# Kernel optimization log

Hardware: AMD Instinct MI355X
Metric: run time of the kernel (lower is better)

Reference implementation:

```python
import jax, jax.numpy as jnp
import numpy as np

N_A, N_B = 50000, 20000   # authors, teams
E0, E1, E2 = 600000, 300000, 300000  # coauthor(A->A), writes(A->B), influences(B->A)
D = 128                   # in_feats = out_feats


def setup_inputs() -> dict:
    key = jax.random.key(0)
    ks = jax.random.split(key, 12)
    h_A = jax.random.normal(ks[0], (N_A, D), jnp.float32)
    h_B = jax.random.normal(ks[1], (N_B, D), jnp.float32)
    W0 = jax.random.normal(ks[2], (D, D), jnp.float32) * 0.05
    W1 = jax.random.normal(ks[3], (D, D), jnp.float32) * 0.05
    W2 = jax.random.normal(ks[4], (D, D), jnp.float32) * 0.05
    b0 = jnp.zeros((D,), jnp.float32)
    b1 = jnp.zeros((D,), jnp.float32)
    b2 = jnp.zeros((D,), jnp.float32)
    src0 = jax.random.randint(ks[5], (E0,), 0, N_A)
    dst0 = jax.random.randint(ks[6], (E0,), 0, N_A)
    src1 = jax.random.randint(ks[7], (E1,), 0, N_A)
    dst1 = jax.random.randint(ks[8], (E1,), 0, N_B)
    src2 = jax.random.randint(ks[9], (E2,), 0, N_B)
    dst2 = jax.random.randint(ks[10], (E2,), 0, N_A)
    return dict(h_A=h_A, h_B=h_B, W0=W0, b0=b0, W1=W1, b1=b1, W2=W2, b2=b2,
                src0=src0, dst0=dst0, src1=src1, dst1=dst1, src2=src2, dst2=dst2)


def _graph_conv(x_src, W, b, src, dst, n_dst):
    """DGL GraphConv, norm='both': out = D_dst^{-1/2} A D_src^{-1/2} (X W) + b."""
    n_src = x_src.shape[0]
    ones = jnp.ones(src.shape[0], x_src.dtype)
    deg_out = jnp.clip(jax.ops.segment_sum(ones, src, num_segments=n_src), 1.0)
    deg_in = jnp.clip(jax.ops.segment_sum(ones, dst, num_segments=n_dst), 1.0)
    m = (x_src @ W) * (deg_out ** -0.5)[:, None]          # [n_src, D]
    agg = jax.ops.segment_sum(m[src], dst, num_segments=n_dst)  # [n_dst, D]
    return agg * (deg_in ** -0.5)[:, None] + b


def reference(h_A, h_B, W0, b0, W1, b1, W2, b2, src0, dst0, src1, dst1, src2, dst2):
    # HeteroGraphConv(aggregate='sum'): sum per-relation GraphConv outputs per dst ntype.
    out_A = (_graph_conv(h_A, W0, b0, src0, dst0, N_A)
             + _graph_conv(h_B, W2, b2, src2, dst2, N_A))
    out_B = _graph_conv(h_A, W1, b1, src1, dst1, N_B)
    # every ntype present in h receives an output, so no passthrough branch fires
    return out_A, out_B
```

## Files before the change

kernel.cpp:

```cpp
#include <hip/hip_runtime.h>

#define NA 50000
#define NB 20000
#define NE0 600000
#define NE1 300000
#define NE2 300000
#define DD 128
#define DEG_TOT (4 * NA + 2 * NB)
#define SUB 32768
#define PER 18750


typedef short bf16x8 __attribute__((ext_vector_type(8)));
typedef float f32x4 __attribute__((ext_vector_type(4)));

__device__ __forceinline__ unsigned short f2bf(float f) {
    union { float f; unsigned int u; } v; v.f = f;
    unsigned int r = v.u + 0x7fffu + ((v.u >> 16) & 1u);
    return (unsigned short)(r >> 16);
}
__device__ __forceinline__ float bf2f(unsigned int u16) {
    union { float f; unsigned int u; } v; v.u = u16 << 16;
    return v.f;
}
__device__ __forceinline__ float lo2f(unsigned int u) {
    union { float f; unsigned int u; } v; v.u = u << 16;
    return v.f;
}
__device__ __forceinline__ float hi2f(unsigned int u) {
    union { float f; unsigned int u; } v; v.u = u & 0xffff0000u;
    return v.f;
}

__global__ __launch_bounds__(1024) void hist_kernel(
    const int* __restrict__ s0, const int* __restrict__ d0,
    const int* __restrict__ s1, const int* __restrict__ d1,
    const int* __restrict__ s2, const int* __restrict__ d2,
    unsigned int* __restrict__ Pd,
    int* __restrict__ rank0, int* __restrict__ rank1, int* __restrict__ rank2)
{
    __shared__ unsigned int h32[SUB / 2];
    const int cfg = blockIdx.z;
    const int En[6] = {NE0, NE0, NE1, NE1, NE2, NE2};
    const int Kn[6] = {NA, NA, NA, NB, NB, NA};
    const int Gn[6] = {32, 32, 16, 16, 16, 16};
    const int Po[6] = {0, 1600000, 3200000, 4000000, 4320000, 4640000};
    int E = En[cfg], K = Kn[cfg], G = Gn[cfg];
    int sub = blockIdx.x, g = blockIdx.y;
    int nsub = (K + SUB - 1) / SUB;
    if (sub >= nsub || g >= G) return;
    const int* keys = cfg == 0 ? s0 : cfg == 1 ? d0 : cfg == 2 ? s1
                    : cfg == 3 ? d1 : cfg == 4 ? s2 : d2;
    int* rk = cfg == 1 ? rank0 : cfg == 3 ? rank1 : cfg == 5 ? rank2 : (int*)0;
    int lo = sub * SUB;
    int hi = min(K, lo + SUB);
    int cnt = hi - lo;
    for (int i = threadIdx.x; i < SUB / 2; i += 1024) h32[i] = 0;
    __syncthreads();
    int e1 = min(E, g * PER + PER);
    for (int e = g * PER + threadIdx.x; e < e1; e += 1024) {
        int k = keys[e];
        if (k >= lo && k < hi) {
            int kk = k - lo;
            unsigned sh = (kk & 1) << 4;
            unsigned old = atomicAdd(&h32[kk >> 1], 1u << sh);
            if (rk) rk[e] = (int)((old >> sh) & 0xffffu);
        }
    }
    __syncthreads();
    unsigned int* outp = Pd + ((Po[cfg] + g * K + lo) >> 1);
    for (int i = threadIdx.x; i < cnt / 2; i += 1024) outp[i] = h32[i];
}

__global__ __launch_bounds__(256) void reduce_kernel(
    const unsigned short* __restrict__ P16, int* __restrict__ ideg,
    float* __restrict__ rdeg)
{
    int i = blockIdx.x * 256 + threadIdx.x;
    if (i >= DEG_TOT) return;
    int h, k;
    if      (i < NA)            { h = 0; k = i; }
    else if (i < 2 * NA)        { h = 1; k = i - NA; }
    else if (i < 3 * NA)        { h = 2; k = i - 2 * NA; }
    else if (i < 3 * NA + NB)   { h = 3; k = i - 3 * NA; }
    else if (i < 3 * NA + 2*NB) { h = 4; k = i - 3 * NA - NB; }
    else                        { h = 5; k = i - 3 * NA - 2 * NB; }
    const int Po[6] = {0, 1600000, 3200000, 4000000, 4320000, 4640000};
    const int Gn[6] = {32, 32, 16, 16, 16, 16};
    const int Kn[6] = {NA, NA, NA, NB, NB, NA};
    const unsigned short* p = P16 + Po[h] + k;
    int K = Kn[h], G = Gn[h], s = 0;
    for (int g = 0; g < G; ++g) s += p[g * K];
    ideg[i] = s;
    rdeg[i] = rsqrtf(fmaxf((float)s, 1.f));
}

__global__ __launch_bounds__(256) void scan_reduce(
    const int* __restrict__ ideg, int* __restrict__ spart)
{
    __shared__ int lds[256];
    int y = blockIdx.y;
    const int off[3] = {NA, 3 * NA, 3 * NA + 2 * NB};
    const int nn[3]  = {NA, NB, NA};
    int n = nn[y];
    int b = blockIdx.x, t = threadIdx.x;
    if (b * 1024 >= n) return;
    const int* deg = ideg + off[y];
    int base = b * 1024 + t * 4;
    int s = 0;
    #pragma unroll
    for (int k = 0; k < 4; ++k) { int i = base + k; if (i < n) s += deg[i]; }
    lds[t] = s; __syncthreads();
    for (int o = 128; o > 0; o >>= 1) {
        if (t < o) lds[t] += lds[t + o];
        __syncthreads();
    }
    if (t == 0) spart[y * 64 + b] = lds[0];
}

__global__ void spine_kernel(int* __restrict__ spart) {
    int w = threadIdx.x >> 6, lane = threadIdx.x & 63;
    const int nblk[3] = {49, 20, 49};
    int n = nblk[w];
    int* p = spart + w * 64;
    int orig = (lane < n) ? p[lane] : 0;
    int v = orig;
    #pragma unroll
    for (int o = 1; o < 64; o <<= 1) {
        int u = __shfl_up(v, o);
        if (lane >= o) v += u;
    }
    if (lane < n) p[lane] = v - orig;
}

__global__ __launch_bounds__(256) void scan_final(
    const int* __restrict__ ideg, const int* __restrict__ spart,
    int* __restrict__ rp)
{
    __shared__ int lds[256];
    int y = blockIdx.y;
    const int off[3] = {NA, 3 * NA, 3 * NA + 2 * NB};
    const int nn[3]  = {NA, NB, NA};
    const int ro[3]  = {0, NA, NA + NB};
    int n = nn[y];
    int b = blockIdx.x, t = threadIdx.x;
    if (b * 1024 >= n) return;
    const int* deg = ideg + off[y];
    int* rowptr = rp + ro[y];
    int base = b * 1024 + t * 4;
    int v[4]; int tsum = 0;
    #pragma unroll
    for (int k = 0; k < 4; ++k) {
        v[k] = (base + k < n) ? deg[base + k] : 0;
        tsum += v[k];
    }
    lds[t] = tsum; __syncthreads();
    for (int o = 1; o < 256; o <<= 1) {
        int x = (t >= o) ? lds[t - o] : 0;
        __syncthreads();
        lds[t] += x;
        __syncthreads();
    }
    int run = lds[t] - tsum + spart[y * 64 + b];
    #pragma unroll
    for (int k = 0; k < 4; ++k) {
        if (base + k < n) rowptr[base + k] = run;
        run += v[k];
    }
}

__global__ __launch_bounds__(256) void offsets_kernel(
    const unsigned short* __restrict__ P16, const int* __restrict__ rp,
    int* __restrict__ O)
{
    int i = blockIdx.x * 256 + threadIdx.x;
    if (i >= 2 * NA + NB) return;
    int pbase, obase, G, K, d, run;
    if (i < NA)           { pbase = 1600000; obase = 0;       G = 32; K = NA; d = i;           run = rp[d]; }
    else if (i < NA + NB) { pbase = 4000000; obase = 1600000; G = 16; K = NB; d = i - NA;      run = rp[NA + d]; }
    else                  { pbase = 4640000; obase = 1920000; G = 16; K = NA; d = i - NA - NB; run = rp[NA + NB + d]; }
    const unsigned short* p = P16 + pbase + d;
    int* o = O + obase + d;
    for (int g = 0; g < G; ++g) {
        int t = p[g * K];
        o[g * K] = run;
        run += t;
    }
}

__global__ __launch_bounds__(512) void place_parallel(
    const int* __restrict__ s0, const int* __restrict__ d0,
    const int* __restrict__ s1, const int* __restrict__ d1,
    const int* __restrict__ s2, const int* __restrict__ d2,
    const int* __restrict__ O,
    const int* __restrict__ rank0, const int* __restrict__ rank1,
    const int* __restrict__ rank2,
    int* __restrict__ csr0, int* __restrict__ csr1, int* __restrict__ csr2)
{
    int z = blockIdx.z;
    const int En[3] = {NE0, NE1, NE2};
    const int Kn[3] = {NA, NB, NA};
    const int Oo[3] = {0, 1600000, 1920000};
    int E = En[z], K = Kn[z];
    const int* src = z == 0 ? s0 : z == 1 ? s1 : s2;
    const int* dst = z == 0 ? d0 : z == 1 ? d1 : d2;
    const int* rk  = z == 0 ? rank0 : z == 1 ? rank1 : rank2;
    int* csr = z == 0 ? csr0 : z == 1 ? csr1 : csr2;
    const int* off = O + Oo[z];
    int e = blockIdx.x * 512 + threadIdx.x;
    if (e >= E) return;
    int d = dst[e];
    int g = e / PER;
    int pos = off[g * K + d] + rk[e];
    csr[pos] = src[e];
}

__global__ __launch_bounds__(256) void wt_kernel(
    const float* __restrict__ W0, const float* __restrict__ W1,
    const float* __restrict__ W2, unsigned short* __restrict__ Wt)
{
    int i = blockIdx.x * 256 + threadIdx.x;
    if (i >= 3 * DD * DD) return;
    int w = i >> 14, r = i & (DD * DD - 1);
    int c = r >> 7, k = r & (DD - 1);
    const float* W = (w == 0) ? W0 : ((w == 1) ? W1 : W2);
    Wt[i] = f2bf(W[k * DD + c]);
}

__global__ __launch_bounds__(256) void gemm_all(
    const float* __restrict__ hA, const float* __restrict__ hB,
    const unsigned short* __restrict__ Wt, const float* __restrict__ rdeg,
    unsigned short* __restrict__ mA0, unsigned short* __restrict__ mA1,
    unsigned short* __restrict__ mB2)
{
    int wid  = threadIdx.x >> 6;
    int lane = threadIdx.x & 63;
    int quad = lane >> 4;
    int l16  = lane & 15;

    if (blockIdx.x < 782) {
        int base = blockIdx.x * 64 + wid * 16;
        if (base >= NA) return;
        int arow = base + l16;
        if (arow >= NA) arow = NA - 1;
        bf16x8 a[4];
        #pragma unroll
        for (int kk = 0; kk < 4; ++kk) {
            const float4* p = (const float4*)(hA + (size_t)arow * DD + kk * 32 + quad * 8);
            float4 u = p[0], w = p[1];
            bf16x8 t;
            t[0] = (short)f2bf(u.x); t[1] = (short)f2bf(u.y);
            t[2] = (short)f2bf(u.z); t[3] = (short)f2bf(u.w);
            t[4] = (short)f2bf(w.x); t[5] = (short)f2bf(w.y);
            t[6] = (short)f2bf(w.z); t[7] = (short)f2bf(w.w);
            a[kk] = t;
        }
        float rs0[4], rs1[4]; int orow0 = base + quad * 4;
        #pragma unroll
        for (int r = 0; r < 4; ++r) {
            int orow = orow0 + r; int c = orow < NA ? orow : 0;
            rs0[r] = rdeg[c]; rs1[r] = rdeg[2 * NA + c];
        }
        #pragma unroll
        for (int ct = 0; ct < 8; ++ct) {
            f32x4 acc0 = {0.f, 0.f, 0.f, 0.f};
            f32x4 acc1 = {0.f, 0.f, 0.f, 0.f};
            const unsigned short* wp = Wt + (size_t)(ct * 16 + l16) * DD + quad * 8;
            #pragma unroll
            for (int kk = 0; kk < 4; ++kk) {
                bf16x8 b0 = *(const bf16x8*)(wp + kk * 32);
                bf16x8 b1 = *(const bf16x8*)(wp + 16384 + kk * 32);
                acc0 = __builtin_amdgcn_mfma_f32_16x16x32_bf16(a[kk], b0, acc0, 0, 0, 0);
                acc1 = __builtin_amdgcn_mfma_f32_16x16x32_bf16(a[kk], b1, acc1, 0, 0, 0);
            }
            #pragma unroll
            for (int r = 0; r < 4; ++r) {
                int orow = orow0 + r;
                if (orow < NA) {
                    mA0[(size_t)orow * DD + ct * 16 + l16] = f2bf(acc0[r] * rs0[r]);
                    mA1[(size_t)orow * DD + ct * 16 + l16] = f2bf(acc1[r] * rs1[r]);
                }
            }
        }
    } else {
        int base = (blockIdx.x - 782) * 64 + wid * 16;
        if (base >= NB) return;
        int arow = base + l16;
        if (arow >= NB) arow = NB - 1;
        bf16x8 a[4];
        #pragma unroll
        for (int kk = 0; kk < 4; ++kk) {
            const float4* p = (const float4*)(hB + (size_t)arow * DD + kk * 32 + quad * 8);
            float4 u = p[0], w = p[1];
            bf16x8 t;
            t[0] = (short)f2bf(u.x); t[1] = (short)f2bf(u.y);
            t[2] = (short)f2bf(u.z); t[3] = (short)f2bf(u.w);
            t[4] = (short)f2bf(w.x); t[5] = (short)f2bf(w.y);
            t[6] = (short)f2bf(w.z); t[7] = (short)f2bf(w.w);
            a[kk] = t;
        }
        float rs[4]; int orow0 = base + quad * 4;
        #pragma unroll
        for (int r = 0; r < 4; ++r) {
            int orow = orow0 + r;
            rs[r] = rdeg[3 * NA + NB + (orow < NB ? orow : 0)];
        }
        #pragma unroll
        for (int ct = 0; ct < 8; ++ct) {
            f32x4 acc = {0.f, 0.f, 0.f, 0.f};
            const unsigned short* wp = Wt + 32768 + (size_t)(ct * 16 + l16) * DD + quad * 8;
            #pragma unroll
            for (int kk = 0; kk < 4; ++kk) {
                bf16x8 b = *(const bf16x8*)(wp + kk * 32);
                acc = __builtin_amdgcn_mfma_f32_16x16x32_bf16(a[kk], b, acc, 0, 0, 0);
            }
            #pragma unroll
            for (int r = 0; r < 4; ++r) {
                int orow = orow0 + r;
                if (orow < NB)
                    mB2[(size_t)orow * DD + ct * 16 + l16] = f2bf(acc[r] * rs[r]);
            }
        }
    }
}

__device__ __forceinline__ void gather_rel(
    const char* __restrict__ Mb, const int* __restrict__ csr,
    int st, int n, int lane, unsigned laneoff, float& o0, float& o1)
{
    for (int ch = 0; ch < n; ch += 64) {
        int m = n - ch; if (m > 64) m = 64;
        int idx = csr[st + ch + (lane < m ? lane : m - 1)];
        int j = 0;
        for (; j + 4 <= m; j += 4) {
            int sA = __shfl(idx, j);
            int sB = __shfl(idx, j + 1);
            int sC = __shfl(idx, j + 2);
            int sD = __shfl(idx, j + 3);
            unsigned uA = *(const unsigned*)(Mb + (((unsigned)sA << 8) + laneoff));
            unsigned uB = *(const unsigned*)(Mb + (((unsigned)sB << 8) + laneoff));
            unsigned uC = *(const unsigned*)(Mb + (((unsigned)sC << 8) + laneoff));
            unsigned uD = *(const unsigned*)(Mb + (((unsigned)sD << 8) + laneoff));
            o0 += lo2f(uA); o1 += hi2f(uA);
            o0 += lo2f(uB); o1 += hi2f(uB);
            o0 += lo2f(uC); o1 += hi2f(uC);
            o0 += lo2f(uD); o1 += hi2f(uD);
        }
        for (; j < m; ++j) {
            int s = __shfl(idx, j);
            unsigned u = *(const unsigned*)(Mb + (((unsigned)s << 8) + laneoff));
            o0 += lo2f(u); o1 += hi2f(u);
        }
    }
}

__global__ __launch_bounds__(256) void gather_all(
    const unsigned short* __restrict__ mA0, const unsigned short* __restrict__ mA1,
    const unsigned short* __restrict__ mB2,
    const int* __restrict__ csr0, const int* __restrict__ csr1,
    const int* __restrict__ csr2,
    const int* __restrict__ rp, const int* __restrict__ ideg,
    const float* __restrict__ rdeg,
    const float* __restrict__ b0, const float* __restrict__ b1,
    const float* __restrict__ b2,
    float* __restrict__ out)
{
    int wid = threadIdx.x >> 6, lane = threadIdx.x & 63;
    unsigned laneoff = (unsigned)lane * 4u;
    int col = lane * 2;

    if (blockIdx.x < 12500) {
        int d = blockIdx.x * 4 + wid;
        float a0 = 0.f, a1 = 0.f, c0 = 0.f, c1 = 0.f;
        gather_rel((const char*)mA0, csr0, rp[d], ideg[NA + d], lane, laneoff, a0, a1);
        gather_rel((const char*)mB2, csr2, rp[NA + NB + d], ideg[3 * NA + 2 * NB + d],
                   lane, laneoff, c0, c1);
        float r0 = rdeg[NA + d], r2 = rdeg[3 * NA + 2 * NB + d];
        float2 o;
        o.x = a0 * r0 + c0 * r2 + b0[col]     + b2[col];
        o.y = a1 * r0 + c1 * r2 + b0[col + 1] + b2[col + 1];
        *(float2*)(out + (size_t)d * DD + col) = o;
    } else {
        int d = (blockIdx.x - 12500) * 4 + wid;
        float a0 = 0.f, a1 = 0.f;
        gather_rel((const char*)mA1, csr1, rp[NA + d], ideg[3 * NA + d],
                   lane, laneoff, a0, a1);
        float r1 = rdeg[3 * NA + d];
        float2 o;
        o.x = a0 * r1 + b1[col];
        o.y = a1 * r1 + b1[col + 1];
        *(float2*)(out + (size_t)(NA + d) * DD + col) = o;
    }
}

extern "C" void kernel_launch(void* const* d_in, const int* in_sizes, int n_in,
                              void* d_out, int out_size, void* d_ws, size_t ws_size,
                              hipStream_t stream) {
    const float* hA = (const float*)d_in[0];
    const float* hB = (const float*)d_in[1];
    const float* W0 = (const float*)d_in[2];
    const float* b0 = (const float*)d_in[3];
    const float* W1 = (const float*)d_in[4];
    const float* b1 = (const float*)d_in[5];
    const float* W2 = (const float*)d_in[6];
    const float* b2 = (const float*)d_in[7];
    const int* s0 = (const int*)d_in[8];
    const int* d0 = (const int*)d_in[9];
    const int* s1 = (const int*)d_in[10];
    const int* d1 = (const int*)d_in[11];
    const int* s2 = (const int*)d_in[12];
    const int* d2 = (const int*)d_in[13];
    float* out = (float*)d_out;
    char* ws = (char*)d_ws;

    unsigned short* mA0 = (unsigned short*)(ws + 0);
    unsigned short* mA1 = (unsigned short*)(ws + 12800000);
    unsigned short* mB2 = (unsigned short*)(ws + 25600000);
    unsigned short* P16 = (unsigned short*)(ws + 0);
    unsigned int*   Pd  = (unsigned int*)(ws + 0);
    int*   O            = (int*)  (ws + 10880000);
    unsigned short* Wt  = (unsigned short*)(ws + 30720000);
    float* rdeg         = (float*)(ws + 30818304);
    int*   ideg         = (int*)  (ws + 31778304);
    int*   rp           = (int*)  (ws + 32738304);
    int*   spart        = (int*)  (ws + 33218304);
    int*   rank0        = (int*)  (ws + 33219328);
    int*   rank1        = (int*)  (ws + 35619328);
    int*   rank2        = (int*)  (ws + 36819328);
    int*   csr0         = (int*)  (ws + 38019328);
    int*   csr1         = (int*)  (ws + 40419328);
    int*   csr2         = (int*)  (ws + 41619328);

    hist_kernel<<<dim3(2, 32, 6), 1024, 0, stream>>>(s0, d0, s1, d1, s2, d2,
                                                     Pd, rank0, rank1, rank2);
    reduce_kernel<<<(DEG_TOT + 255) / 256, 256, 0, stream>>>(P16, ideg, rdeg);

    scan_reduce<<<dim3(49, 3), 256, 0, stream>>>(ideg, spart);
    spine_kernel<<<1, 192, 0, stream>>>(spart);
    scan_final<<<dim3(49, 3), 256, 0, stream>>>(ideg, spart, rp);

    offsets_kernel<<<(2 * NA + NB + 255) / 256, 256, 0, stream>>>(P16, rp, O);
    place_parallel<<<dim3((NE0 + 511) / 512, 1, 3), 512, 0, stream>>>(
        s0, d0, s1, d1, s2, d2, O, rank0, rank1, rank2, csr0, csr1, csr2);

    wt_kernel<<<(3 * DD * DD + 255) / 256, 256, 0, stream>>>(W0, W1, W2, Wt);
    gemm_all<<<782 + 313, 256, 0, stream>>>(hA, hB, Wt, rdeg, mA0, mA1, mB2);

    gather_all<<<12500 + 5000, 256, 0, stream>>>(mA0, mA1, mB2,
        csr0, csr1, csr2, rp, ideg, rdeg, b0, b1, b2, out);
}
```

Measured before the change: 264.7 us.

## Fuse preprocessing kernels and widen gather loads to 16-byte rows per quarter-wave

Folds the weight transpose/convert into an extra z-slice of the histogram kernel. It merges degree reduction with the scan partial sums, and merges the scan spine and per-group offsets into the final scan, cutting the launch count from nine to five. The gather kernel now has each 16-lane quarter of a wave load a full 256-byte bf16 row with uint4 loads, processing four edges at once, then reduces the quarters with shuffles. This trades fewer launches and wider memory transactions for a redundant spine prefix in every block and the extra cross-lane reduction.

Result: slower. 276.9 us (+4.6%).

```diff
diff --git a/kernel.cpp b/kernel.cpp
--- a/kernel.cpp
+++ b/kernel.cpp
@@ -19,10 +19,6 @@
     unsigned int r = v.u + 0x7fffu + ((v.u >> 16) & 1u);
     return (unsigned short)(r >> 16);
 }
-__device__ __forceinline__ float bf2f(unsigned int u16) {
-    union { float f; unsigned int u; } v; v.u = u16 << 16;
-    return v.f;
-}
 __device__ __forceinline__ float lo2f(unsigned int u) {
     union { float f; unsigned int u; } v; v.u = u << 16;
     return v.f;
@@ -37,10 +33,22 @@
     const int* __restrict__ s1, const int* __restrict__ d1,
     const int* __restrict__ s2, const int* __restrict__ d2,
     unsigned int* __restrict__ Pd,
-    int* __restrict__ rank0, int* __restrict__ rank1, int* __restrict__ rank2)
+    int* __restrict__ rank0, int* __restrict__ rank1, int* __restrict__ rank2,
+    const float* __restrict__ W0, const float* __restrict__ W1,
+    const float* __restrict__ W2, unsigned short* __restrict__ Wt)
 {
     __shared__ unsigned int h32[SUB / 2];
     const int cfg = blockIdx.z;
+    if (cfg == 6) {
+        int flat = blockIdx.y * 2 + blockIdx.x;
+        if (flat >= 48) return;
+        int i = flat * 1024 + threadIdx.x;
+        int w = i >> 14, r = i & (DD * DD - 1);
+        int c = r >> 7, k = r & (DD - 1);
+        const float* W = (w == 0) ? W0 : ((w == 1) ? W1 : W2);
+        Wt[i] = f2bf(W[k * DD + c]);
+        return;
+    }
     const int En[6] = {NE0, NE0, NE1, NE1, NE2, NE2};
     const int Kn[6] = {NA, NA, NA, NB, NB, NA};
     const int Gn[6] = {32, 32, 16, 16, 16, 16};
@@ -72,81 +80,67 @@
     for (int i = threadIdx.x; i < cnt / 2; i += 1024) outp[i] = h32[i];
 }
 
-__global__ __launch_bounds__(256) void reduce_kernel(
+__global__ __launch_bounds__(256) void reduce2(
     const unsigned short* __restrict__ P16, int* __restrict__ ideg,
-    float* __restrict__ rdeg)
-{
-    int i = blockIdx.x * 256 + threadIdx.x;
-    if (i >= DEG_TOT) return;
-    int h, k;
-    if      (i < NA)            { h = 0; k = i; }
-    else if (i < 2 * NA)        { h = 1; k = i - NA; }
-    else if (i < 3 * NA)        { h = 2; k = i - 2 * NA; }
-    else if (i < 3 * NA + NB)   { h = 3; k = i - 3 * NA; }
-    else if (i < 3 * NA + 2*NB) { h = 4; k = i - 3 * NA - NB; }
-    else                        { h = 5; k = i - 3 * NA - 2 * NB; }
+    float* __restrict__ rdeg, int* __restrict__ spart)
+{
+    __shared__ int lds[256];
+    const int y = blockIdx.y;
+    const int Ro[6] = {0, NA, 2 * NA, 3 * NA, 3 * NA + NB, 3 * NA + 2 * NB};
+    const int Kr[6] = {NA, NA, NA, NB, NB, NA};
+    const int Gr[6] = {32, 32, 16, 16, 16, 16};
     const int Po[6] = {0, 1600000, 3200000, 4000000, 4320000, 4640000};
-    const int Gn[6] = {32, 32, 16, 16, 16, 16};
-    const int Kn[6] = {NA, NA, NA, NB, NB, NA};
-    const unsigned short* p = P16 + Po[h] + k;
-    int K = Kn[h], G = Gn[h], s = 0;
-    for (int g = 0; g < G; ++g) s += p[g * K];
-    ideg[i] = s;
-    rdeg[i] = rsqrtf(fmaxf((float)s, 1.f));
-}
-
-__global__ __launch_bounds__(256) void scan_reduce(
-    const int* __restrict__ ideg, int* __restrict__ spart)
+    int K = Kr[y], G = Gr[y];
+    int b = blockIdx.x, t = threadIdx.x;
+    if (b * 1024 >= K) return;
+    int base = b * 1024 + t * 4;
+    int tsum = 0;
+    #pragma unroll
+    for (int k = 0; k < 4; ++k) {
+        int key = base + k;
+        if (key < K) {
+            const unsigned short* p = P16 + Po[y] + key;
+            int s = 0;
+            for (int g = 0; g < G; ++g) s += p[g * K];
+            ideg[Ro[y] + key] = s;
+            rdeg[Ro[y] + key] = rsqrtf(fmaxf((float)s, 1.f));
+            tsum += s;
+        }
+    }
+    if (y == 1 || y == 3 || y == 5) {
+        int slot = (y - 1) >> 1;
+        lds[t] = tsum; __syncthreads();
+        for (int o = 128; o > 0; o >>= 1) {
+            if (t < o) lds[t] += lds[t + o];
+            __syncthreads();
+        }
+        if (t == 0) spart[slot * 64 + b] = lds[0];
+    }
+}
+
+__global__ __launch_bounds__(256) void scan_final2(
+    const int* __restrict__ ideg, const int* __restrict__ spart,
+    const unsigned short* __restrict__ P16,
+    int* __restrict__ rp, int* __restrict__ O)
 {
     __shared__ int lds[256];
-    int y = blockIdx.y;
-    const int off[3] = {NA, 3 * NA, 3 * NA + 2 * NB};
-    const int nn[3]  = {NA, NB, NA};
-    int n = nn[y];
+    const int y = blockIdx.y;
+    const int off[3]   = {NA, 3 * NA, 3 * NA + 2 * NB};
+    const int nn[3]    = {NA, NB, NA};
+    const int ro[3]    = {0, NA, NA + NB};
+    const int pbase[3] = {1600000, 4000000, 4640000};
+    const int obase[3] = {0, 1600000, 1920000};
+    const int Gd[3]    = {32, 16, 16};
+    int n = nn[y], K = n, G = Gd[y];
     int b = blockIdx.x, t = threadIdx.x;
     if (b * 1024 >= n) return;
+    int lane = t & 63;
+
+    int pv = (lane < b) ? spart[y * 64 + lane] : 0;
+    #pragma unroll
+    for (int o = 32; o > 0; o >>= 1) pv += __shfl_xor(pv, o);
+
     const int* deg = ideg + off[y];
-    int base = b * 1024 + t * 4;
-    int s = 0;
-    #pragma unroll
-    for (int k = 0; k < 4; ++k) { int i = base + k; if (i < n) s += deg[i]; }
-    lds[t] = s; __syncthreads();
-    for (int o = 128; o > 0; o >>= 1) {
-        if (t < o) lds[t] += lds[t + o];
-        __syncthreads();
-    }
-    if (t == 0) spart[y * 64 + b] = lds[0];
-}
-
-__global__ void spine_kernel(int* __restrict__ spart) {
-    int w = threadIdx.x >> 6, lane = threadIdx.x & 63;
-    const int nblk[3] = {49, 20, 49};
-    int n = nblk[w];
-    int* p = spart + w * 64;
-    int orig = (lane < n) ? p[lane] : 0;
-    int v = orig;
-    #pragma unroll
-    for (int o = 1; o < 64; o <<= 1) {
-        int u = __shfl_up(v, o);
-        if (lane >= o) v += u;
-    }
-    if (lane < n) p[lane] = v - orig;
-}
-
-__global__ __launch_bounds__(256) void scan_final(
-    const int* __restrict__ ideg, const int* __restrict__ spart,
-    int* __restrict__ rp)
-{
-    __shared__ int lds[256];
-    int y = blockIdx.y;
-    const int off[3] = {NA, 3 * NA, 3 * NA + 2 * NB};
-    const int nn[3]  = {NA, NB, NA};
-    const int ro[3]  = {0, NA, NA + NB};
-    int n = nn[y];
-    int b = blockIdx.x, t = threadIdx.x;
-    if (b * 1024 >= n) return;
-    const int* deg = ideg + off[y];
-    int* rowptr = rp + ro[y];
     int base = b * 1024 + t * 4;
     int v[4]; int tsum = 0;
     #pragma unroll
@@ -161,30 +155,22 @@
         lds[t] += x;
         __syncthreads();
     }
-    int run = lds[t] - tsum + spart[y * 64 + b];
+    int run = lds[t] - tsum + pv;
+    int* rowptr = rp + ro[y];
+    const unsigned short* pb = P16 + pbase[y];
+    int* ob = O + obase[y];
     #pragma unroll
     for (int k = 0; k < 4; ++k) {
-        if (base + k < n) rowptr[base + k] = run;
-        run += v[k];
-    }
-}
-
-__global__ __launch_bounds__(256) void offsets_kernel(
-    const unsigned short* __restrict__ P16, const int* __restrict__ rp,
-    int* __restrict__ O)
-{
-    int i = blockIdx.x * 256 + threadIdx.x;
-    if (i >= 2 * NA + NB) return;
-    int pbase, obase, G, K, d, run;
-    if (i < NA)           { pbase = 1600000; obase = 0;       G = 32; K = NA; d = i;           run = rp[d]; }
-    else if (i < NA + NB) { pbase = 4000000; obase = 1600000; G = 16; K = NB; d = i - NA;      run = rp[NA + d]; }
-    else                  { pbase = 4640000; obase = 1920000; G = 16; K = NA; d = i - NA - NB; run = rp[NA + NB + d]; }
-    const unsigned short* p = P16 + pbase + d;
-    int* o = O + obase + d;
-    for (int g = 0; g < G; ++g) {
-        int t = p[g * K];
-        o[g * K] = run;
-        run += t;
+        int key = base + k;
+        if (key < n) {
+            rowptr[key] = run;
+            int r2 = run;
+            for (int g = 0; g < G; ++g) {
+                ob[g * K + key] = r2;
+                r2 += pb[g * K + key];
+            }
+            run += v[k];
+        }
     }
 }
 
@@ -213,18 +199,6 @@
     int g = e / PER;
     int pos = off[g * K + d] + rk[e];
     csr[pos] = src[e];
-}
-
-__global__ __launch_bounds__(256) void wt_kernel(
-    const float* __restrict__ W0, const float* __restrict__ W1,
-    const float* __restrict__ W2, unsigned short* __restrict__ Wt)
-{
-    int i = blockIdx.x * 256 + threadIdx.x;
-    if (i >= 3 * DD * DD) return;
-    int w = i >> 14, r = i & (DD * DD - 1);
-    int c = r >> 7, k = r & (DD - 1);
-    const float* W = (w == 0) ? W0 : ((w == 1) ? W1 : W2);
-    Wt[i] = f2bf(W[k * DD + c]);
 }
 
 __global__ __launch_bounds__(256) void gemm_all(
@@ -324,32 +298,42 @@
     }
 }
 
-__device__ __forceinline__ void gather_rel(
+__device__ __forceinline__ void acc8(float* o, uint4 u) {
+    o[0] += lo2f(u.x); o[1] += hi2f(u.x);
+    o[2] += lo2f(u.y); o[3] += hi2f(u.y);
+    o[4] += lo2f(u.z); o[5] += hi2f(u.z);
+    o[6] += lo2f(u.w); o[7] += hi2f(u.w);
+}
+__device__ __forceinline__ void gather_rel4(
     const char* __restrict__ Mb, const int* __restrict__ csr,
-    int st, int n, int lane, unsigned laneoff, float& o0, float& o1)
+    int st, int n, int lane, int q, unsigned laneoff, float* o)
 {
     for (int ch = 0; ch < n; ch += 64) {
         int m = n - ch; if (m > 64) m = 64;
         int idx = csr[st + ch + (lane < m ? lane : m - 1)];
         int j = 0;
-        for (; j + 4 <= m; j += 4) {
-            int sA = __shfl(idx, j);
-            int sB = __shfl(idx, j + 1);
-            int sC = __shfl(idx, j + 2);
-            int sD = __shfl(idx, j + 3);
-            unsigned uA = *(const unsigned*)(Mb + (((unsigned)sA << 8) + laneoff));
-            unsigned uB = *(const unsigned*)(Mb + (((unsigned)sB << 8) + laneoff));
-            unsigned uC = *(const unsigned*)(Mb + (((unsigned)sC << 8) + laneoff));
-            unsigned uD = *(const unsigned*)(Mb + (((unsigned)sD << 8) + laneoff));
-            o0 += lo2f(uA); o1 += hi2f(uA);
-            o0 += lo2f(uB); o1 += hi2f(uB);
-            o0 += lo2f(uC); o1 += hi2f(uC);
-            o0 += lo2f(uD); o1 += hi2f(uD);
-        }
-        for (; j < m; ++j) {
-            int s = __shfl(idx, j);
-            unsigned u = *(const unsigned*)(Mb + (((unsigned)s << 8) + laneoff));
-            o0 += lo2f(u); o1 += hi2f(u);
+        for (; j + 8 <= m; j += 8) {
+            int sA = __shfl(idx, j + q);
+            int sB = __shfl(idx, j + 4 + q);
+            uint4 uA = *(const uint4*)(Mb + (((unsigned)sA << 8) + laneoff));
+            uint4 uB = *(const uint4*)(Mb + (((unsigned)sB << 8) + laneoff));
+            acc8(o, uA); acc8(o, uB);
+        }
+        if (j + 4 <= m) {
+            int s = __shfl(idx, j + q);
+            uint4 u = *(const uint4*)(Mb + (((unsigned)s << 8) + laneoff));
+            acc8(o, u);
+            j += 4;
+        }
+        if (j < m) {
+            int jj = j + q;
+            float w = jj < m ? 1.f : 0.f;
+            int s = __shfl(idx, jj < m ? jj : m - 1);
+            uint4 u = *(const uint4*)(Mb + (((unsigned)s << 8) + laneoff));
+            o[0] = fmaf(w, lo2f(u.x), o[0]); o[1] = fmaf(w, hi2f(u.x), o[1]);
+            o[2] = fmaf(w, lo2f(u.y), o[2]); o[3] = fmaf(w, hi2f(u.y), o[3]);
+            o[4] = fmaf(w, lo2f(u.z), o[4]); o[5] = fmaf(w, hi2f(u.z), o[5]);
+            o[6] = fmaf(w, lo2f(u.w), o[6]); o[7] = fmaf(w, hi2f(u.w), o[7]);
         }
     }
 }
@@ -366,30 +350,57 @@
     float* __restrict__ out)
 {
     int wid = threadIdx.x >> 6, lane = threadIdx.x & 63;
-    unsigned laneoff = (unsigned)lane * 4u;
-    int col = lane * 2;
+    int q = lane >> 4, l16 = lane & 15;
+    unsigned laneoff = (unsigned)l16 * 16u;
+    float v[8];
+    #pragma unroll
+    for (int i = 0; i < 8; ++i) v[i] = 0.f;
+    float* op;
+    const float *bia, *bib;
 
     if (blockIdx.x < 12500) {
         int d = blockIdx.x * 4 + wid;
-        float a0 = 0.f, a1 = 0.f, c0 = 0.f, c1 = 0.f;
-        gather_rel((const char*)mA0, csr0, rp[d], ideg[NA + d], lane, laneoff, a0, a1);
-        gather_rel((const char*)mB2, csr2, rp[NA + NB + d], ideg[3 * NA + 2 * NB + d],
-                   lane, laneoff, c0, c1);
+        float c[8];
+        #pragma unroll
+        for (int i = 0; i < 8; ++i) c[i] = 0.f;
+        gather_rel4((const char*)mA0, csr0, rp[d], ideg[NA + d], lane, q, laneoff, v);
+        gather_rel4((const char*)mB2, csr2, rp[NA + NB + d], ideg[3 * NA + 2 * NB + d],
+                    lane, q, laneoff, c);
         float r0 = rdeg[NA + d], r2 = rdeg[3 * NA + 2 * NB + d];
-        float2 o;
-        o.x = a0 * r0 + c0 * r2 + b0[col]     + b2[col];
-        o.y = a1 * r0 + c1 * r2 + b0[col + 1] + b2[col + 1];
-        *(float2*)(out + (size_t)d * DD + col) = o;
+        #pragma unroll
+        for (int i = 0; i < 8; ++i) v[i] = v[i] * r0 + c[i] * r2;
+        op = out + (size_t)d * DD;
+        bia = b0; bib = b2;
     } else {
         int d = (blockIdx.x - 12500) * 4 + wid;
-        float a0 = 0.f, a1 = 0.f;
-        gather_rel((const char*)mA1, csr1, rp[NA + d], ideg[3 * NA + d],
-                   lane, laneoff, a0, a1);
+        gather_rel4((const char*)mA1, csr1, rp[NA + d], ideg[3 * NA + d],
+                    lane, q, laneoff, v);
         float r1 = rdeg[3 * NA + d];
-        float2 o;
-        o.x = a0 * r1 + b1[col];
-        o.y = a1 * r1 + b1[col + 1];
-        *(float2*)(out + (size_t)(NA + d) * DD + col) = o;
+        #pragma unroll
+        for (int i = 0; i < 8; ++i) v[i] *= r1;
+        op = out + (size_t)(NA + d) * DD;
+        bia = b1; bib = 0;
+    }
+
+    #pragma unroll
+    for (int i = 0; i < 8; ++i) {
+        v[i] += __shfl_down(v[i], 32);
+        v[i] += __shfl_down(v[i], 16);
+    }
+    if (lane < 16) {
+        int col = l16 * 8;
+        float4 ba0 = *(const float4*)(bia + col);
+        float4 ba1 = *(const float4*)(bia + col + 4);
+        if (bib) {
+            float4 bb0 = *(const float4*)(bib + col);
+            float4 bb1 = *(const float4*)(bib + col + 4);
+            ba0.x += bb0.x; ba0.y += bb0.y; ba0.z += bb0.z; ba0.w += bb0.w;
+            ba1.x += bb1.x; ba1.y += bb1.y; ba1.z += bb1.z; ba1.w += bb1.w;
+        }
+        float4 o0 = {v[0] + ba0.x, v[1] + ba0.y, v[2] + ba0.z, v[3] + ba0.w};
+        float4 o1 = {v[4] + ba1.x, v[5] + ba1.y, v[6] + ba1.z, v[7] + ba1.w};
+        *(float4*)(op + col) = o0;
+        *(float4*)(op + col + 4) = o1;
     }
 }
 
@@ -431,21 +442,13 @@
     int*   csr1         = (int*)  (ws + 40419328);
     int*   csr2         = (int*)  (ws + 41619328);
 
-    hist_kernel<<<dim3(2, 32, 6), 1024, 0, stream>>>(s0, d0, s1, d1, s2, d2,
-                                                     Pd, rank0, rank1, rank2);
-    reduce_kernel<<<(DEG_TOT + 255) / 256, 256, 0, stream>>>(P16, ideg, rdeg);
-
-    scan_reduce<<<dim3(49, 3), 256, 0, stream>>>(ideg, spart);
-    spine_kernel<<<1, 192, 0, stream>>>(spart);
-    scan_final<<<dim3(49, 3), 256, 0, stream>>>(ideg, spart, rp);
-
-    offsets_kernel<<<(2 * NA + NB + 255) / 256, 256, 0, stream>>>(P16, rp, O);
+    hist_kernel<<<dim3(2, 32, 7), 1024, 0, stream>>>(s0, d0, s1, d1, s2, d2,
+        Pd, rank0, rank1, rank2, W0, W1, W2, Wt);
+    reduce2<<<dim3(49, 6), 256, 0, stream>>>(P16, ideg, rdeg, spart);
+    scan_final2<<<dim3(49, 3), 256, 0, stream>>>(ideg, spart, P16, rp, O);
     place_parallel<<<dim3((NE0 + 511) / 512, 1, 3), 512, 0, stream>>>(
         s0, d0, s1, d1, s2, d2, O, rank0, rank1, rank2, csr0, csr1, csr2);
-
-    wt_kernel<<<(3 * DD * DD + 255) / 256, 256, 0, stream>>>(W0, W1, W2, Wt);
     gemm_all<<<782 + 313, 256, 0, stream>>>(hA, hB, Wt, rdeg, mA0, mA1, mB2);
-
     gather_all<<<12500 + 5000, 256, 0, stream>>>(mA0, mA1, mB2,
         csr0, csr1, csr2, rp, ideg, rdeg, b0, b1, b2, out);
 }
```
